# Kernel tuning notes

Measured on AMD Instinct MI355X. Metric: run time of the kernel, lower is better.

## Reference

```python
import jax, jax.numpy as jnp
import numpy as np

N_CUST, N_PROD, D, H, OUT, E = 100000, 10000, 128, 128, 64, 500000
RELS = ["purchase", "redeem", "transfer_to", "transfer_from", "dividend_from"]


def setup_inputs() -> dict:
    key = jax.random.key(0)
    ks = jax.random.split(key, 40)
    inp = {}
    inp["x_cust"] = jax.random.normal(ks[0], (N_CUST, D), jnp.float32)
    inp["x_prod"] = jax.random.normal(ks[1], (N_PROD, D), jnp.float32)
    for i, r in enumerate(RELS):
        inp["src_" + r] = jax.random.randint(ks[2 + 2 * i], (E,), 0, N_CUST)
        inp["dst_" + r] = jax.random.randint(ks[3 + 2 * i], (E,), 0, N_PROD)
    s = 0.05
    names = [("W_gcn", (D, H)), ("b_gcn", (H,)), ("Ws_gat", (D, H)), ("Wd_gat", (D, H)),
             ("a_s_gat", (H,)), ("a_d_gat", (H,)), ("b_gat", (H,)),
             ("Wl_to", (D, H)), ("b_to", (H,)), ("Wr_to", (D, H)),
             ("Wl_from", (D, H)), ("b_from", (H,)), ("Wr_from", (D, H)),
             ("Wl_div", (D, H)), ("b_div", (H,)), ("Wr_div", (D, H)),
             ("W_out", (H, OUT)), ("b_out", (OUT,))]
    for i, (n, shp) in enumerate(names):
        inp[n] = jax.random.normal(ks[12 + i], shp, jnp.float32) * s
    return inp


def _gcn(x_src, src, dst, W, b):
    # symmetric-norm bipartite GCN: transform then gather->scale->scatter
    deg_s = jax.ops.segment_sum(jnp.ones_like(src, jnp.float32), src, N_CUST)
    deg_d = jax.ops.segment_sum(jnp.ones_like(dst, jnp.float32), dst, N_PROD)
    norm = jax.lax.rsqrt(deg_s[src] * deg_d[dst])  # [E]
    h = x_src @ W  # [N_CUST, H]
    return jax.ops.segment_sum(norm[:, None] * h[src], dst, N_PROD) + b


def _gat(x_src, x_dst, src, dst, Ws, Wd, a_s, a_d, b):
    # single-head bipartite GAT with edge-softmax over incoming edges at dst
    hs = x_src @ Ws                     # [N_CUST, H]
    ls = hs @ a_s                       # [N_CUST]
    ld = (x_dst @ Wd) @ a_d             # [N_PROD]
    logit = jax.nn.leaky_relu(ls[src] + ld[dst], 0.2)  # [E]
    m = jax.ops.segment_max(logit, dst, N_PROD)
    e = jnp.exp(logit - m[dst])
    den = jax.ops.segment_sum(e, dst, N_PROD)
    alpha = e / den[dst]
    return jax.ops.segment_sum(alpha[:, None] * hs[src], dst, N_PROD) + b


def _sage(x_src, x_dst, src, dst, Wl, bl, Wr):
    # mean-aggregate raw src features, then linear; plus root transform of dst
    s = jax.ops.segment_sum(x_src[src], dst, N_PROD)
    c = jax.ops.segment_sum(jnp.ones_like(dst, jnp.float32), dst, N_PROD)
    mean = s / jnp.maximum(c, 1.0)[:, None]
    return mean @ Wl + bl + x_dst @ Wr


def reference(x_cust, x_prod, src_purchase, dst_purchase, src_redeem, dst_redeem,
              src_transfer_to, dst_transfer_to, src_transfer_from, dst_transfer_from,
              src_dividend_from, dst_dividend_from,
              W_gcn, b_gcn, Ws_gat, Wd_gat, a_s_gat, a_d_gat, b_gat,
              Wl_to, b_to, Wr_to, Wl_from, b_from, Wr_from, Wl_div, b_div, Wr_div,
              W_out, b_out):
    prod = _gcn(x_cust, src_purchase, dst_purchase, W_gcn, b_gcn)
    prod = prod + _gat(x_cust, x_prod, src_redeem, dst_redeem, Ws_gat, Wd_gat, a_s_gat, a_d_gat, b_gat)
    prod = prod + _sage(x_cust, x_prod, src_transfer_to, dst_transfer_to, Wl_to, b_to, Wr_to)
    prod = prod + _sage(x_cust, x_prod, src_transfer_from, dst_transfer_from, Wl_from, b_from, Wr_from)
    prod = prod + _sage(x_cust, x_prod, src_dividend_from, dst_dividend_from, Wl_div, b_div, Wr_div)
    prod = jax.nn.relu(prod)  # HeteroConv(aggr='sum') then relu
    return prod @ W_out + b_out  # [N_PROD, OUT]
```

## Files before the change

### kernel.cpp

```cpp
#include <hip/hip_runtime.h>

#define WF 64
#define CAP 128
#define CH 2048
#define LC 32
#define NGMAX 160
#define BINCAP 3584

typedef int v4i __attribute__((ext_vector_type(4)));

#if __has_builtin(__builtin_amdgcn_cvt_f32_fp8) && __has_builtin(__builtin_amdgcn_cvt_pk_fp8_f32)
#define HW_FP8 1
#endif

__device__ __forceinline__ unsigned fp8enc1(float x) {
    unsigned b = __builtin_bit_cast(unsigned, x);
    unsigned s = (b >> 24) & 0x80u;
    int E = (b >> 23) & 0xff;
    unsigned m = b & 0x7fffffu;
    unsigned mr = (m + 0x7ffffu + ((m >> 20) & 1u)) >> 20;
    int e8 = E - 120 + (int)(mr >> 3);
    mr &= 7u;
    if (e8 <= 0) return s;
    if (e8 > 15) { e8 = 15; mr = 7u; }
    return s | ((unsigned)e8 << 3) | mr;
}
__device__ __forceinline__ float fp8dec1(unsigned u8) {
    unsigned f = ((u8 & 0x80u) << 24) | (((u8 & 0x7fu) << 20) + 0x3C000000u);
    return (u8 & 0x7fu) ? __builtin_bit_cast(float, f) : 0.f;
}
__device__ __forceinline__ unsigned fp8pack4(float4 u) {
#ifdef HW_FP8
    int r = __builtin_amdgcn_cvt_pk_fp8_f32(u.x, u.y, 0, false);
    r = __builtin_amdgcn_cvt_pk_fp8_f32(u.z, u.w, r, true);
    return (unsigned)r;
#else
    return fp8enc1(u.x) | (fp8enc1(u.y) << 8) | (fp8enc1(u.z) << 16) | (fp8enc1(u.w) << 24);
#endif
}
__device__ __forceinline__ void accP(float w, unsigned u,
                                     float& a0, float& a1, float& a2, float& a3) {
#ifdef HW_FP8
    a0 = fmaf(w, __builtin_amdgcn_cvt_f32_fp8((int)u, 0), a0);
    a1 = fmaf(w, __builtin_amdgcn_cvt_f32_fp8((int)u, 1), a1);
    a2 = fmaf(w, __builtin_amdgcn_cvt_f32_fp8((int)u, 2), a2);
    a3 = fmaf(w, __builtin_amdgcn_cvt_f32_fp8((int)u, 3), a3);
#else
    a0 = fmaf(w, fp8dec1(u & 0xffu), a0);
    a1 = fmaf(w, fp8dec1((u >> 8) & 0xffu), a1);
    a2 = fmaf(w, fp8dec1((u >> 16) & 0xffu), a2);
    a3 = fmaf(w, fp8dec1(u >> 24), a3);
#endif
}

__global__ void k_init(int* deg_s, int nc2, int* bincur, int nb, int ZB,
                       const float* __restrict__ Ws, const float* __restrict__ Wd,
                       const float* __restrict__ as_, const float* __restrict__ ad_,
                       const float* __restrict__ bg, const float* __restrict__ bga,
                       const float* __restrict__ bto, const float* __restrict__ bfr,
                       const float* __restrict__ bdv,
                       const float* __restrict__ Wrt, const float* __restrict__ Wrf,
                       const float* __restrict__ Wrd,
                       float* vs, float* vd, float* bsum, float* Wrsum) {
    int b = blockIdx.x, t = threadIdx.x;
    if (b < ZB) {
        int i = b * 256 + t;
        if (i < nc2) deg_s[i] = 0;
        if (i < nb) bincur[i] = 0;
    } else if (b < ZB + 64) {
        int i = (b - ZB) * 256 + t;
        Wrsum[i] = Wrt[i] + Wrf[i] + Wrd[i];
    } else {
        if (t < 128) {
            float a = 0.f, bb = 0.f;
            for (int h = 0; h < 128; ++h) {
                a += Ws[t * 128 + h] * as_[h];
                bb += Wd[t * 128 + h] * ad_[h];
            }
            vs[t] = a; vd[t] = bb;
            bsum[t] = bg[t] + bga[t] + bto[t] + bfr[t] + bdv[t];
        }
    }
}

__global__ __launch_bounds__(256) void k_bin(
    const int* s0, const int* s1, const int* s2, const int* s3, const int* s4,
    const int* d0, const int* d1, const int* d2, const int* d3, const int* d4,
    int* bincur, int* gbin, int* deg_s, int E, int NP, int ng,
    int bpjE, int B0, int HB4, int CB,
    const float* __restrict__ xc, const float* __restrict__ xp,
    const float* __restrict__ vs, const float* __restrict__ vd,
    unsigned* __restrict__ xh, float* __restrict__ lsb, float* __restrict__ ldb,
    int NC) {
    __shared__ int lcnt[NGMAX];
    __shared__ int lbase[NGMAX];
    __shared__ int lbin[NGMAX * LC];
    int b = blockIdx.x, t = threadIdx.x;
    if (b < B0) {
        int rel = b / bpjE;
        int blk = b - rel * bpjE;
        const int *sp, *dp;
        switch (rel) {
            case 0: sp = s0; dp = d0; break;
            case 1: sp = s1; dp = d1; break;
            case 2: sp = s2; dp = d2; break;
            case 3: sp = s3; dp = d3; break;
            default: sp = s4; dp = d4; break;
        }
        for (int i = t; i < ng; i += 256) lcnt[i] = 0;
        __syncthreads();
        int* bc = bincur + rel * ng;
        int* gb0 = gbin + (size_t)rel * ng * BINCAP;
        int start = blk * CH;
        int q0 = start + t * 8;
#pragma unroll
        for (int c = 0; c < 8; c += 4) {
            int q = q0 + c;
            if (q >= E) break;
            if (q + 3 < E) {
                v4i dv = __builtin_nontemporal_load((const v4i*)(dp + q));
                v4i sv = __builtin_nontemporal_load((const v4i*)(sp + q));
                int dd[4] = {dv.x, dv.y, dv.z, dv.w};
                int ss[4] = {sv.x, sv.y, sv.z, sv.w};
#pragma unroll
                for (int z = 0; z < 4; ++z) {
                    int bin = dd[z] >> 6;
                    int pk = (ss[z] << 6) | (dd[z] & 63);
                    int pos = atomicAdd(&lcnt[bin], 1);
                    if (pos < LC) lbin[bin * LC + pos] = pk;
                    else {
                        int g = atomicAdd(bc + bin, 1);
                        if (g < BINCAP) gb0[(size_t)bin * BINCAP + g] = pk;
                    }
                }
            } else {
                for (int i = q; i < E; ++i) {
                    int d = dp[i];
                    int bin = d >> 6;
                    int pk = (sp[i] << 6) | (d & 63);
                    int pos = atomicAdd(&lcnt[bin], 1);
                    if (pos < LC) lbin[bin * LC + pos] = pk;
                    else {
                        int g = atomicAdd(bc + bin, 1);
                        if (g < BINCAP) gb0[(size_t)bin * BINCAP + g] = pk;
                    }
                }
            }
        }
        __syncthreads();
        if (t < ng) {
            int c = min(lcnt[t], LC);
            lbase[t] = atomicAdd(bc + t, c);
        }
        __syncthreads();
        int wv = t >> 6, lane = t & 63;
        for (int bin = wv; bin < ng; bin += 4) {
            int c = min(lcnt[bin], LC);
            int gbase = lbase[bin];
            int* gp = gb0 + (size_t)bin * BINCAP;
            for (int i = lane; i < c; i += 64) {
                int g = gbase + i;
                if (g < BINCAP) gp[g] = lbin[bin * LC + i];
            }
        }
    } else if (b < B0 + HB4) {
        int q = ((b - B0) * 256 + t) * 4;
        if (q >= E) return;
        if (q + 3 < E) {
            v4i v = __builtin_nontemporal_load((const v4i*)(s0 + q));
            atomicAdd(deg_s + v.x, 1); atomicAdd(deg_s + v.y, 1);
            atomicAdd(deg_s + v.z, 1); atomicAdd(deg_s + v.w, 1);
        } else {
            for (int i = q; i < E; ++i) atomicAdd(deg_s + s0[i], 1);
        }
    } else if (b < B0 + HB4 + CB) {
        int row = (b - B0 - HB4) * 8 + (t >> 5);
        int q = t & 31;
        if (row >= NC) return;
        float4 u = *(const float4*)(xc + (size_t)row * 128 + 4 * q);
        float4 v = *(const float4*)(vs + 4 * q);
        float s = u.x * v.x + u.y * v.y + u.z * v.z + u.w * v.w;
        xh[(size_t)row * 32 + q] = fp8pack4(u);
#pragma unroll
        for (int o = 16; o; o >>= 1) s += __shfl_xor(s, o, WF);
        if (q == 0) lsb[row] = s;
    } else {
        int row = (b - B0 - HB4 - CB) * 4 + (t >> 6);
        int l = t & 63;
        if (row >= NP) return;
        const float* xr = xp + (size_t)row * 128;
        float s = xr[2 * l] * vd[2 * l] + xr[2 * l + 1] * vd[2 * l + 1];
        for (int o = 32; o; o >>= 1) s += __shfl_down(s, o, WF);
        if (l == 0) ldb[row] = s;
    }
}

__global__ __launch_bounds__(256) void k_aggf(
    const int* __restrict__ gbin, const int* __restrict__ bincur,
    const int* __restrict__ deg_s,
    const float* __restrict__ ls, const float* __restrict__ ld,
    const unsigned* __restrict__ xh,
    float* __restrict__ aggG, float* __restrict__ aggA, float* __restrict__ aggM,
    int NP, int ng) {
    __shared__ int cnt[16];
    __shared__ int buck[16][CAP + 1];
    __shared__ float wbuf[4][CAP + 1];
    int t = threadIdx.x;
    int rel = blockIdx.x / (4 * ng);
    int rem = blockIdx.x - rel * 4 * ng;
    int grp = rem >> 2, sub = rem & 3;
    if (t < 16) cnt[t] = 0;
    __syncthreads();
    int binid = rel * ng + grp;
    int n = min(bincur[binid], BINCAP);
    const int* bsrc = gbin + (size_t)binid * BINCAP;
    for (int i = t; i < n; i += 256) {
        int e = bsrc[i];
        int lp = e & 63;
        if ((lp >> 4) == sub) {
            int li = lp & 15;
            int pos = atomicAdd(&cnt[li], 1);
            if (pos < CAP) buck[li][pos] = e >> 6;
        }
    }
    __syncthreads();
    if (t < 16) buck[t][min(cnt[t], CAP)] = 0;
    __syncthreads();

    int wv = t >> 6, l = t & 63;
    int half = l >> 5, q = l & 31;

    for (int r = 0; r < 4; ++r) {
        int li = r * 4 + wv;
        int p = grp * 64 + sub * 16 + li;
        bool valid = (p < NP);
        int m = valid ? min(cnt[li], CAP) : 0;

        if (rel == 0) {
            float rd = rsqrtf((float)m);
            for (int e = l; e < m; e += WF)
                wbuf[wv][e] = rsqrtf((float)deg_s[buck[li][e]]) * rd;
        } else if (rel == 1) {
            if (m > 0) {
                float ldp = ld[p];
                float ml = -3.4e38f, dl = 0.f;
                for (int e = l; e < m; e += WF) {
                    float tt = ls[buck[li][e]] + ldp;
                    tt = tt > 0.f ? tt : 0.2f * tt;
                    wbuf[wv][e] = tt;
                    if (tt > ml) { dl = dl * __expf(ml - tt) + 1.f; ml = tt; }
                    else dl += __expf(tt - ml);
                }
                for (int o = 32; o; o >>= 1) {
                    float m2 = __shfl_xor(ml, o, WF), d2 = __shfl_xor(dl, o, WF);
                    float mm = fmaxf(ml, m2);
                    dl = dl * __expf(ml - mm) + d2 * __expf(m2 - mm);
                    ml = mm;
                }
                float inv = 1.f / dl;
                for (int e = l; e < m; e += WF)
                    wbuf[wv][e] = __expf(wbuf[wv][e] - ml) * inv;
            }
        } else {
            float sc = 1.f / fmaxf((float)m, 1.f);
            for (int e = l; e < m; e += WF) wbuf[wv][e] = sc;
        }
        if (l == 0) wbuf[wv][m] = 0.f;
        __builtin_amdgcn_wave_barrier();

        float a0 = 0.f, a1 = 0.f, a2 = 0.f, a3 = 0.f;
        int npairs = (m + 1) >> 1;
        int j = 0;
        for (; j + 8 <= npairs; j += 8) {
            int ss[8]; float wk[8]; unsigned uu[8];
#pragma unroll
            for (int z = 0; z < 8; ++z) {
                int e = 2 * (j + z) + half;
                ss[z] = buck[li][e];
                wk[z] = wbuf[wv][e];
            }
#pragma unroll
            for (int z = 0; z < 8; ++z)
                uu[z] = xh[(size_t)ss[z] * 32 + q];
#pragma unroll
            for (int z = 0; z < 8; ++z)
                accP(wk[z], uu[z], a0, a1, a2, a3);
        }
        for (; j < npairs; ++j) {
            int e = 2 * j + half;
            int s0 = buck[li][e];
            float w0 = wbuf[wv][e];
            unsigned u0 = xh[(size_t)s0 * 32 + q];
            accP(w0, u0, a0, a1, a2, a3);
        }

        a0 += __shfl_xor(a0, 32, WF);
        a1 += __shfl_xor(a1, 32, WF);
        a2 += __shfl_xor(a2, 32, WF);
        a3 += __shfl_xor(a3, 32, WF);

        if (valid && l < 32) {
            float* dst;
            if (rel == 0)      dst = aggG + (size_t)p * 128;
            else if (rel == 1) dst = aggA + (size_t)p * 128;
            else               dst = aggM + ((size_t)(rel - 2) * NP + p) * 128;
            *(float4*)(dst + 4 * q) = make_float4(a0, a1, a2, a3);
        }
    }
}

__global__ __launch_bounds__(256) void k_gemm_out(
    const float* __restrict__ A0, const float* __restrict__ A1, const float* __restrict__ A2,
    const float* __restrict__ A3, const float* __restrict__ A4, const float* __restrict__ A5,
    const float* __restrict__ W0, const float* __restrict__ W1, const float* __restrict__ W2,
    const float* __restrict__ W3, const float* __restrict__ W4, const float* __restrict__ W5,
    const float* __restrict__ bsum, const float* __restrict__ Wout,
    const float* __restrict__ bout, float* __restrict__ out, int NP) {
    __shared__ float xs[16][128];
    __shared__ float ts[16][128];
    int row0 = blockIdx.x * 16, tid = threadIdx.x;
    int cg = (tid & 31) * 4;
    int rg = tid >> 5;
    float acc0[4] = {0.f, 0.f, 0.f, 0.f};
    float acc1[4] = {0.f, 0.f, 0.f, 0.f};
    const float* Af[6] = {A0, A1, A2, A3, A4, A5};
    const float* Wm[6] = {W0, W1, W2, W3, W4, W5};
    int r = tid >> 4, c = (tid & 15) * 8;
    for (int m = 0; m < 6; ++m) {
        __syncthreads();
        {
            const float* A = Af[m] + (size_t)(row0 + r) * 128 + c;
            float4 u0 = *(const float4*)A;
            float4 u1 = *(const float4*)(A + 4);
            *(float4*)&xs[r][c] = u0;
            *(float4*)&xs[r][c + 4] = u1;
        }
        __syncthreads();
        const float* W = Wm[m];
        for (int k = 0; k < 128; k += 4) {
            float4 a0 = *(const float4*)&xs[2 * rg][k];
            float4 a1 = *(const float4*)&xs[2 * rg + 1][k];
            float4 w0 = *(const float4*)(W + (k + 0) * 128 + cg);
            float4 w1 = *(const float4*)(W + (k + 1) * 128 + cg);
            float4 w2 = *(const float4*)(W + (k + 2) * 128 + cg);
            float4 w3 = *(const float4*)(W + (k + 3) * 128 + cg);
            acc0[0] = fmaf(a0.x, w0.x, acc0[0]); acc0[1] = fmaf(a0.x, w0.y, acc0[1]);
            acc0[2] = fmaf(a0.x, w0.z, acc0[2]); acc0[3] = fmaf(a0.x, w0.w, acc0[3]);
            acc1[0] = fmaf(a1.x, w0.x, acc1[0]); acc1[1] = fmaf(a1.x, w0.y, acc1[1]);
            acc1[2] = fmaf(a1.x, w0.z, acc1[2]); acc1[3] = fmaf(a1.x, w0.w, acc1[3]);
            acc0[0] = fmaf(a0.y, w1.x, acc0[0]); acc0[1] = fmaf(a0.y, w1.y, acc0[1]);
            acc0[2] = fmaf(a0.y, w1.z, acc0[2]); acc0[3] = fmaf(a0.y, w1.w, acc0[3]);
            acc1[0] = fmaf(a1.y, w1.x, acc1[0]); acc1[1] = fmaf(a1.y, w1.y, acc1[1]);
            acc1[2] = fmaf(a1.y, w1.z, acc1[2]); acc1[3] = fmaf(a1.y, w1.w, acc1[3]);
            acc0[0] = fmaf(a0.z, w2.x, acc0[0]); acc0[1] = fmaf(a0.z, w2.y, acc0[1]);
            acc0[2] = fmaf(a0.z, w2.z, acc0[2]); acc0[3] = fmaf(a0.z, w2.w, acc0[3]);
            acc1[0] = fmaf(a1.z, w2.x, acc1[0]); acc1[1] = fmaf(a1.z, w2.y, acc1[1]);
            acc1[2] = fmaf(a1.z, w2.z, acc1[2]); acc1[3] = fmaf(a1.z, w2.w, acc1[3]);
            acc0[0] = fmaf(a0.w, w3.x, acc0[0]); acc0[1] = fmaf(a0.w, w3.y, acc0[1]);
            acc0[2] = fmaf(a0.w, w3.z, acc0[2]); acc0[3] = fmaf(a0.w, w3.w, acc0[3]);
            acc1[0] = fmaf(a1.w, w3.x, acc1[0]); acc1[1] = fmaf(a1.w, w3.y, acc1[1]);
            acc1[2] = fmaf(a1.w, w3.z, acc1[2]); acc1[3] = fmaf(a1.w, w3.w, acc1[3]);
        }
    }
    float4 bb = *(const float4*)(bsum + cg);
    {
        float v0 = acc0[0] + bb.x, v1 = acc0[1] + bb.y, v2 = acc0[2] + bb.z, v3 = acc0[3] + bb.w;
        ts[2 * rg][cg + 0] = v0 > 0.f ? v0 : 0.f;
        ts[2 * rg][cg + 1] = v1 > 0.f ? v1 : 0.f;
        ts[2 * rg][cg + 2] = v2 > 0.f ? v2 : 0.f;
        ts[2 * rg][cg + 3] = v3 > 0.f ? v3 : 0.f;
        v0 = acc1[0] + bb.x; v1 = acc1[1] + bb.y; v2 = acc1[2] + bb.z; v3 = acc1[3] + bb.w;
        ts[2 * rg + 1][cg + 0] = v0 > 0.f ? v0 : 0.f;
        ts[2 * rg + 1][cg + 1] = v1 > 0.f ? v1 : 0.f;
        ts[2 * rg + 1][cg + 2] = v2 > 0.f ? v2 : 0.f;
        ts[2 * rg + 1][cg + 3] = v3 > 0.f ? v3 : 0.f;
    }
    __syncthreads();
    int o = tid & 63, rb = tid >> 6;
    float o0 = 0.f, o1 = 0.f, o2 = 0.f, o3 = 0.f;
    for (int k = 0; k < 128; k += 2) {
        float wa = Wout[k * 64 + o], wb = Wout[(k + 1) * 64 + o];
        o0 = fmaf(ts[rb][k], wa, fmaf(ts[rb][k + 1], wb, o0));
        o1 = fmaf(ts[rb + 4][k], wa, fmaf(ts[rb + 4][k + 1], wb, o1));
        o2 = fmaf(ts[rb + 8][k], wa, fmaf(ts[rb + 8][k + 1], wb, o2));
        o3 = fmaf(ts[rb + 12][k], wa, fmaf(ts[rb + 12][k + 1], wb, o3));
    }
    float bo = bout[o];
    out[(size_t)(row0 + rb) * 64 + o]      = o0 + bo;
    out[(size_t)(row0 + rb + 4) * 64 + o]  = o1 + bo;
    out[(size_t)(row0 + rb + 8) * 64 + o]  = o2 + bo;
    out[(size_t)(row0 + rb + 12) * 64 + o] = o3 + bo;
}

extern "C" void kernel_launch(void* const* d_in, const int* in_sizes, int n_in,
                              void* d_out, int out_size, void* d_ws, size_t ws_size,
                              hipStream_t stream) {
    const float* x_cust = (const float*)d_in[0];
    const float* x_prod = (const float*)d_in[1];
    const int* src_pur = (const int*)d_in[2];  const int* dst_pur = (const int*)d_in[3];
    const int* src_red = (const int*)d_in[4];  const int* dst_red = (const int*)d_in[5];
    const int* src_to  = (const int*)d_in[6];  const int* dst_to  = (const int*)d_in[7];
    const int* src_fr  = (const int*)d_in[8];  const int* dst_fr  = (const int*)d_in[9];
    const int* src_dv  = (const int*)d_in[10]; const int* dst_dv  = (const int*)d_in[11];
    const float* W_gcn = (const float*)d_in[12];
    const float* b_gcn = (const float*)d_in[13];
    const float* Ws_gat = (const float*)d_in[14]; const float* Wd_gat = (const float*)d_in[15];
    const float* a_s = (const float*)d_in[16]; const float* a_d = (const float*)d_in[17];
    const float* b_gat = (const float*)d_in[18];
    const float* Wl_to = (const float*)d_in[19]; const float* b_to = (const float*)d_in[20];
    const float* Wr_to = (const float*)d_in[21];
    const float* Wl_fr = (const float*)d_in[22]; const float* b_fr = (const float*)d_in[23];
    const float* Wr_fr = (const float*)d_in[24];
    const float* Wl_dv = (const float*)d_in[25]; const float* b_dv = (const float*)d_in[26];
    const float* Wr_dv = (const float*)d_in[27];
    const float* W_out = (const float*)d_in[28]; const float* b_out = (const float*)d_in[29];
    float* out = (float*)d_out;

    int NC = in_sizes[0] / 128;
    int NP = in_sizes[1] / 128;
    int E  = in_sizes[2];
    int ng = (NP + 63) >> 6;

    char* ws = (char*)d_ws;
    size_t off = 0;
    auto alloc = [&](size_t bytes) -> void* {
        void* p = ws + off;
        off = (off + bytes + 255) & ~(size_t)255;
        return p;
    };
    int*      deg_s  = (int*)alloc((size_t)NC * 4);
    int*      bincur = (int*)alloc((size_t)5 * NGMAX * 4);
    int*      gbin   = (int*)alloc((size_t)5 * NGMAX * BINCAP * 4);
    float*    lsb    = (float*)alloc((size_t)NC * 4);
    float*    ldb    = (float*)alloc((size_t)NP * 4);
    float*    vs     = (float*)alloc(512);
    float*    vd     = (float*)alloc(512);
    float*    bsum   = (float*)alloc(512);
    float*    Wrsum  = (float*)alloc(128 * 128 * 4);
    unsigned* xh     = (unsigned*)alloc((size_t)NC * 32 * 4);
    float*    aggG   = (float*)alloc((size_t)5 * NP * 128 * 4);
    float*    aggA   = aggG + (size_t)NP * 128;
    float*    aggM   = aggG + (size_t)2 * NP * 128;

    int ZB = (NC + 255) / 256;
    k_init<<<ZB + 64 + 1, 256, 0, stream>>>(deg_s, NC, bincur, 5 * ng, ZB,
                                            Ws_gat, Wd_gat, a_s, a_d,
                                            b_gcn, b_gat, b_to, b_fr, b_dv,
                                            Wr_to, Wr_fr, Wr_dv,
                                            vs, vd, bsum, Wrsum);

    int bpjE = (E + CH - 1) / CH;
    int bpj4 = ((E + 3) / 4 + 255) / 256;
    int B0 = 5 * bpjE, HB4 = bpj4, CB = (NC + 7) / 8, PB = (NP + 3) / 4;
    k_bin<<<B0 + HB4 + CB + PB, 256, 0, stream>>>(
        src_pur, src_red, src_to, src_fr, src_dv,
        dst_pur, dst_red, dst_to, dst_fr, dst_dv,
        bincur, gbin, deg_s, E, NP, ng, bpjE, B0, HB4, CB,
        x_cust, x_prod, vs, vd, xh, lsb, ldb, NC);

    k_aggf<<<5 * ng * 4, 256, 0, stream>>>(gbin, bincur, deg_s, lsb, ldb, xh,
                                           aggG, aggA, aggM, NP, ng);

    k_gemm_out<<<NP / 16, 256, 0, stream>>>(aggG, aggA, aggM, aggM + (size_t)NP * 128,
                                            aggM + (size_t)2 * NP * 128, x_prod,
                                            W_gcn, Ws_gat, Wl_to, Wl_fr, Wl_dv, Wrsum,
                                            bsum, W_out, b_out, out, NP);
}
```

Baseline: 322.2 us.

## Use split-bf16 MFMA for output GEMMs with pretransposed weights

Replaces the scalar FP32 FMA GEMM in k_gemm_out with bf16 MFMA 16x16x32 instructions. Each FP32 value is split into hi and lo bf16 parts and three MFMAs are issued per tile to keep near-FP32 accuracy. k_init now transposes and splits the six concatenated layer weights and W_out into bf16 hi/lo buffers, and the tile grows to 32 rows per block. This moves the dense transform and output projection onto matrix cores, at the cost of split arithmetic and extra preprocessing.

```diff
diff --git a/kernel.cpp b/kernel.cpp
--- a/kernel.cpp
+++ b/kernel.cpp
@@ -8,6 +8,8 @@
 #define BINCAP 3584
 
 typedef int v4i __attribute__((ext_vector_type(4)));
+typedef short short8 __attribute__((ext_vector_type(8)));
+typedef float f32x4 __attribute__((ext_vector_type(4)));
 
 #if __has_builtin(__builtin_amdgcn_cvt_f32_fp8) && __has_builtin(__builtin_amdgcn_cvt_pk_fp8_f32)
 #define HW_FP8 1
@@ -53,24 +55,36 @@
 #endif
 }
 
+__device__ __forceinline__ short bf16r(float x) {
+    unsigned u = __builtin_bit_cast(unsigned, x);
+    u += 0x7fffu + ((u >> 16) & 1u);
+    return (short)(u >> 16);
+}
+__device__ __forceinline__ void bfsplit(float x, short& hi, short& lo) {
+    unsigned u = __builtin_bit_cast(unsigned, x);
+    hi = (short)(u >> 16);
+    float fh = __builtin_bit_cast(float, u & 0xffff0000u);
+    lo = bf16r(x - fh);
+}
+
 __global__ void k_init(int* deg_s, int nc2, int* bincur, int nb, int ZB,
                        const float* __restrict__ Ws, const float* __restrict__ Wd,
                        const float* __restrict__ as_, const float* __restrict__ ad_,
                        const float* __restrict__ bg, const float* __restrict__ bga,
                        const float* __restrict__ bto, const float* __restrict__ bfr,
                        const float* __restrict__ bdv,
+                       const float* __restrict__ Wg, const float* __restrict__ Wlt,
+                       const float* __restrict__ Wlf, const float* __restrict__ Wld,
                        const float* __restrict__ Wrt, const float* __restrict__ Wrf,
-                       const float* __restrict__ Wrd,
-                       float* vs, float* vd, float* bsum, float* Wrsum) {
+                       const float* __restrict__ Wrd, const float* __restrict__ Wo,
+                       float* vs, float* vd, float* bsum,
+                       short* wth, short* wtl, short* woth, short* wotl) {
     int b = blockIdx.x, t = threadIdx.x;
     if (b < ZB) {
         int i = b * 256 + t;
         if (i < nc2) deg_s[i] = 0;
         if (i < nb) bincur[i] = 0;
-    } else if (b < ZB + 64) {
-        int i = (b - ZB) * 256 + t;
-        Wrsum[i] = Wrt[i] + Wrf[i] + Wrd[i];
-    } else {
+    } else if (b == ZB) {
         if (t < 128) {
             float a = 0.f, bb = 0.f;
             for (int h = 0; h < 128; ++h) {
@@ -80,6 +94,30 @@
             vs[t] = a; vd[t] = bb;
             bsum[t] = bg[t] + bga[t] + bto[t] + bfr[t] + bdv[t];
         }
+    } else if (b < ZB + 385) {
+        int e = (b - ZB - 1) * 256 + t;
+        int h = e / 768;
+        int q = e - h * 768;
+        int m = q >> 7, k = q & 127;
+        int src = k * 128 + h;
+        float val;
+        switch (m) {
+            case 0: val = Wg[src]; break;
+            case 1: val = Ws[src]; break;
+            case 2: val = Wlt[src]; break;
+            case 3: val = Wlf[src]; break;
+            case 4: val = Wld[src]; break;
+            default: val = Wrt[src] + Wrf[src] + Wrd[src]; break;
+        }
+        short hi, lo;
+        bfsplit(val, hi, lo);
+        wth[e] = hi; wtl[e] = lo;
+    } else {
+        int e = (b - ZB - 385) * 256 + t;
+        int o = e >> 7, k = e & 127;
+        short hi, lo;
+        bfsplit(Wo[k * 64 + o], hi, lo);
+        woth[e] = hi; wotl[e] = lo;
     }
 }
 
@@ -312,84 +350,98 @@
 __global__ __launch_bounds__(256) void k_gemm_out(
     const float* __restrict__ A0, const float* __restrict__ A1, const float* __restrict__ A2,
     const float* __restrict__ A3, const float* __restrict__ A4, const float* __restrict__ A5,
-    const float* __restrict__ W0, const float* __restrict__ W1, const float* __restrict__ W2,
-    const float* __restrict__ W3, const float* __restrict__ W4, const float* __restrict__ W5,
-    const float* __restrict__ bsum, const float* __restrict__ Wout,
-    const float* __restrict__ bout, float* __restrict__ out, int NP) {
-    __shared__ float xs[16][128];
-    __shared__ float ts[16][128];
-    int row0 = blockIdx.x * 16, tid = threadIdx.x;
-    int cg = (tid & 31) * 4;
-    int rg = tid >> 5;
-    float acc0[4] = {0.f, 0.f, 0.f, 0.f};
-    float acc1[4] = {0.f, 0.f, 0.f, 0.f};
+    const short* __restrict__ wth, const short* __restrict__ wtl,
+    const short* __restrict__ woth, const short* __restrict__ wotl,
+    const float* __restrict__ bsum, const float* __restrict__ bout,
+    float* __restrict__ out, int NP) {
+    __shared__ short c1h[32][136];
+    __shared__ short c1l[32][136];
+    int t = threadIdx.x;
+    int w = t >> 6, l = t & 63;
+    int wr = w >> 1, wc = w & 1;
+    int lr = l & 15, lq = l >> 4;
+    int kq = lq * 8;
+    int row0 = blockIdx.x * 32;
     const float* Af[6] = {A0, A1, A2, A3, A4, A5};
-    const float* Wm[6] = {W0, W1, W2, W3, W4, W5};
-    int r = tid >> 4, c = (tid & 15) * 8;
+
+    f32x4 acc[4] = {};
+    int ar = row0 + 16 * wr + lr;
+    if (ar > NP - 1) ar = NP - 1;
+
+#pragma unroll
     for (int m = 0; m < 6; ++m) {
-        __syncthreads();
-        {
-            const float* A = Af[m] + (size_t)(row0 + r) * 128 + c;
-            float4 u0 = *(const float4*)A;
-            float4 u1 = *(const float4*)(A + 4);
-            *(float4*)&xs[r][c] = u0;
-            *(float4*)&xs[r][c + 4] = u1;
-        }
-        __syncthreads();
-        const float* W = Wm[m];
-        for (int k = 0; k < 128; k += 4) {
-            float4 a0 = *(const float4*)&xs[2 * rg][k];
-            float4 a1 = *(const float4*)&xs[2 * rg + 1][k];
-            float4 w0 = *(const float4*)(W + (k + 0) * 128 + cg);
-            float4 w1 = *(const float4*)(W + (k + 1) * 128 + cg);
-            float4 w2 = *(const float4*)(W + (k + 2) * 128 + cg);
-            float4 w3 = *(const float4*)(W + (k + 3) * 128 + cg);
-            acc0[0] = fmaf(a0.x, w0.x, acc0[0]); acc0[1] = fmaf(a0.x, w0.y, acc0[1]);
-            acc0[2] = fmaf(a0.x, w0.z, acc0[2]); acc0[3] = fmaf(a0.x, w0.w, acc0[3]);
-            acc1[0] = fmaf(a1.x, w0.x, acc1[0]); acc1[1] = fmaf(a1.x, w0.y, acc1[1]);
-            acc1[2] = fmaf(a1.x, w0.z, acc1[2]); acc1[3] = fmaf(a1.x, w0.w, acc1[3]);
-            acc0[0] = fmaf(a0.y, w1.x, acc0[0]); acc0[1] = fmaf(a0.y, w1.y, acc0[1]);
-            acc0[2] = fmaf(a0.y, w1.z, acc0[2]); acc0[3] = fmaf(a0.y, w1.w, acc0[3]);
-            acc1[0] = fmaf(a1.y, w1.x, acc1[0]); acc1[1] = fmaf(a1.y, w1.y, acc1[1]);
-            acc1[2] = fmaf(a1.y, w1.z, acc1[2]); acc1[3] = fmaf(a1.y, w1.w, acc1[3]);
-            acc0[0] = fmaf(a0.z, w2.x, acc0[0]); acc0[1] = fmaf(a0.z, w2.y, acc0[1]);
-            acc0[2] = fmaf(a0.z, w2.z, acc0[2]); acc0[3] = fmaf(a0.z, w2.w, acc0[3]);
-            acc1[0] = fmaf(a1.z, w2.x, acc1[0]); acc1[1] = fmaf(a1.z, w2.y, acc1[1]);
-            acc1[2] = fmaf(a1.z, w2.z, acc1[2]); acc1[3] = fmaf(a1.z, w2.w, acc1[3]);
-            acc0[0] = fmaf(a0.w, w3.x, acc0[0]); acc0[1] = fmaf(a0.w, w3.y, acc0[1]);
-            acc0[2] = fmaf(a0.w, w3.z, acc0[2]); acc0[3] = fmaf(a0.w, w3.w, acc0[3]);
-            acc1[0] = fmaf(a1.w, w3.x, acc1[0]); acc1[1] = fmaf(a1.w, w3.y, acc1[1]);
-            acc1[2] = fmaf(a1.w, w3.z, acc1[2]); acc1[3] = fmaf(a1.w, w3.w, acc1[3]);
-        }
-    }
-    float4 bb = *(const float4*)(bsum + cg);
-    {
-        float v0 = acc0[0] + bb.x, v1 = acc0[1] + bb.y, v2 = acc0[2] + bb.z, v3 = acc0[3] + bb.w;
-        ts[2 * rg][cg + 0] = v0 > 0.f ? v0 : 0.f;
-        ts[2 * rg][cg + 1] = v1 > 0.f ? v1 : 0.f;
-        ts[2 * rg][cg + 2] = v2 > 0.f ? v2 : 0.f;
-        ts[2 * rg][cg + 3] = v3 > 0.f ? v3 : 0.f;
-        v0 = acc1[0] + bb.x; v1 = acc1[1] + bb.y; v2 = acc1[2] + bb.z; v3 = acc1[3] + bb.w;
-        ts[2 * rg + 1][cg + 0] = v0 > 0.f ? v0 : 0.f;
-        ts[2 * rg + 1][cg + 1] = v1 > 0.f ? v1 : 0.f;
-        ts[2 * rg + 1][cg + 2] = v2 > 0.f ? v2 : 0.f;
-        ts[2 * rg + 1][cg + 3] = v3 > 0.f ? v3 : 0.f;
+        const float* ap = Af[m] + (size_t)ar * 128;
+#pragma unroll
+        for (int kk = 0; kk < 4; ++kk) {
+            int koff = kk * 32 + kq;
+            float4 u0 = *(const float4*)(ap + koff);
+            float4 u1 = *(const float4*)(ap + koff + 4);
+            float uf[8] = {u0.x, u0.y, u0.z, u0.w, u1.x, u1.y, u1.z, u1.w};
+            short8 ah, al;
+#pragma unroll
+            for (int j = 0; j < 8; ++j) {
+                short hh, ll;
+                bfsplit(uf[j], hh, ll);
+                ah[j] = hh; al[j] = ll;
+            }
+            int kbase = m * 128 + kk * 32 + kq;
+#pragma unroll
+            for (int ci = 0; ci < 4; ++ci) {
+                int hcol = 64 * wc + 16 * ci + lr;
+                short8 bh = *(const short8*)(wth + (size_t)hcol * 768 + kbase);
+                short8 bl = *(const short8*)(wtl + (size_t)hcol * 768 + kbase);
+                acc[ci] = __builtin_amdgcn_mfma_f32_16x16x32_bf16(ah, bh, acc[ci], 0, 0, 0);
+                acc[ci] = __builtin_amdgcn_mfma_f32_16x16x32_bf16(al, bh, acc[ci], 0, 0, 0);
+                acc[ci] = __builtin_amdgcn_mfma_f32_16x16x32_bf16(ah, bl, acc[ci], 0, 0, 0);
+            }
+        }
+    }
+
+#pragma unroll
+    for (int ci = 0; ci < 4; ++ci) {
+        int col = 64 * wc + 16 * ci + lr;
+        float bs = bsum[col];
+#pragma unroll
+        for (int r = 0; r < 4; ++r) {
+            float v = acc[ci][r] + bs;
+            v = v > 0.f ? v : 0.f;
+            short hh, ll;
+            bfsplit(v, hh, ll);
+            int rl = 16 * wr + 4 * lq + r;
+            c1h[rl][col] = hh;
+            c1l[rl][col] = ll;
+        }
     }
     __syncthreads();
-    int o = tid & 63, rb = tid >> 6;
-    float o0 = 0.f, o1 = 0.f, o2 = 0.f, o3 = 0.f;
-    for (int k = 0; k < 128; k += 2) {
-        float wa = Wout[k * 64 + o], wb = Wout[(k + 1) * 64 + o];
-        o0 = fmaf(ts[rb][k], wa, fmaf(ts[rb][k + 1], wb, o0));
-        o1 = fmaf(ts[rb + 4][k], wa, fmaf(ts[rb + 4][k + 1], wb, o1));
-        o2 = fmaf(ts[rb + 8][k], wa, fmaf(ts[rb + 8][k + 1], wb, o2));
-        o3 = fmaf(ts[rb + 12][k], wa, fmaf(ts[rb + 12][k + 1], wb, o3));
-    }
-    float bo = bout[o];
-    out[(size_t)(row0 + rb) * 64 + o]      = o0 + bo;
-    out[(size_t)(row0 + rb + 4) * 64 + o]  = o1 + bo;
-    out[(size_t)(row0 + rb + 8) * 64 + o]  = o2 + bo;
-    out[(size_t)(row0 + rb + 12) * 64 + o] = o3 + bo;
+
+    f32x4 acc2[2] = {};
+    int r16 = 16 * (w >> 1);
+    int oc0 = 32 * (w & 1);
+#pragma unroll
+    for (int kb2 = 0; kb2 < 4; ++kb2) {
+        int kof = kb2 * 32 + kq;
+        short8 a2h = *(const short8*)&c1h[r16 + lr][kof];
+        short8 a2l = *(const short8*)&c1l[r16 + lr][kof];
+#pragma unroll
+        for (int nb = 0; nb < 2; ++nb) {
+            int o = oc0 + 16 * nb + lr;
+            short8 b2h = *(const short8*)(woth + o * 128 + kof);
+            short8 b2l = *(const short8*)(wotl + o * 128 + kof);
+            acc2[nb] = __builtin_amdgcn_mfma_f32_16x16x32_bf16(a2h, b2h, acc2[nb], 0, 0, 0);
+            acc2[nb] = __builtin_amdgcn_mfma_f32_16x16x32_bf16(a2l, b2h, acc2[nb], 0, 0, 0);
+            acc2[nb] = __builtin_amdgcn_mfma_f32_16x16x32_bf16(a2h, b2l, acc2[nb], 0, 0, 0);
+        }
+    }
+#pragma unroll
+    for (int nb = 0; nb < 2; ++nb) {
+        int col = oc0 + 16 * nb + lr;
+        float bo = bout[col];
+#pragma unroll
+        for (int r = 0; r < 4; ++r) {
+            int row = row0 + r16 + 4 * lq + r;
+            if (row < NP) out[(size_t)row * 64 + col] = acc2[nb][r] + bo;
+        }
+    }
 }
 
 extern "C" void kernel_launch(void* const* d_in, const int* in_sizes, int n_in,
@@ -436,18 +488,22 @@
     float*    vs     = (float*)alloc(512);
     float*    vd     = (float*)alloc(512);
     float*    bsum   = (float*)alloc(512);
-    float*    Wrsum  = (float*)alloc(128 * 128 * 4);
+    short*    wth    = (short*)alloc((size_t)98304 * 2);
+    short*    wtl    = (short*)alloc((size_t)98304 * 2);
+    short*    woth   = (short*)alloc((size_t)8192 * 2);
+    short*    wotl   = (short*)alloc((size_t)8192 * 2);
     unsigned* xh     = (unsigned*)alloc((size_t)NC * 32 * 4);
     float*    aggG   = (float*)alloc((size_t)5 * NP * 128 * 4);
     float*    aggA   = aggG + (size_t)NP * 128;
     float*    aggM   = aggG + (size_t)2 * NP * 128;
 
     int ZB = (NC + 255) / 256;
-    k_init<<<ZB + 64 + 1, 256, 0, stream>>>(deg_s, NC, bincur, 5 * ng, ZB,
-                                            Ws_gat, Wd_gat, a_s, a_d,
-                                            b_gcn, b_gat, b_to, b_fr, b_dv,
-                                            Wr_to, Wr_fr, Wr_dv,
-                                            vs, vd, bsum, Wrsum);
+    k_init<<<ZB + 1 + 384 + 32, 256, 0, stream>>>(deg_s, NC, bincur, 5 * ng, ZB,
+                                                  Ws_gat, Wd_gat, a_s, a_d,
+                                                  b_gcn, b_gat, b_to, b_fr, b_dv,
+                                                  W_gcn, Wl_to, Wl_fr, Wl_dv,
+                                                  Wr_to, Wr_fr, Wr_dv, W_out,
+                                                  vs, vd, bsum, wth, wtl, woth, wotl);
 
     int bpjE = (E + CH - 1) / CH;
     int bpj4 = ((E + 3) / 4 + 255) / 256;
@@ -461,8 +517,7 @@
     k_aggf<<<5 * ng * 4, 256, 0, stream>>>(gbin, bincur, deg_s, lsb, ldb, xh,
                                            aggG, aggA, aggM, NP, ng);
 
-    k_gemm_out<<<NP / 16, 256, 0, stream>>>(aggG, aggA, aggM, aggM + (size_t)NP * 128,
-                                            aggM + (size_t)2 * NP * 128, x_prod,
-                                            W_gcn, Ws_gat, Wl_to, Wl_fr, Wl_dv, Wrsum,
-                                            bsum, W_out, b_out, out, NP);
-}
+    k_gemm_out<<<(NP + 31) / 32, 256, 0, stream>>>(
+        aggG, aggA, aggM, aggM + (size_t)NP * 128, aggM + (size_t)2 * NP * 128, x_prod,
+        wth, wtl, woth, wotl, bsum, b_out, out, NP);
+}
```

After: 305.7 us. 1.05x faster.
